# Kernel optimization log

Measured on AMD Instinct MI355X. Metric: run time of the kernel, lower is better.

## Reference

```python
import jax, jax.numpy as jnp
import numpy as np

B, S, D, H = 2, 2048, 1024, 16
HD = D // H

def setup_inputs() -> dict:
    key = jax.random.key(0)
    ks = jax.random.split(key, 6)
    X = jax.random.normal(ks[0], (B, S, D), dtype=jnp.float32)
    mask = jax.random.randint(ks[1], (B, 1, S, S), 0, 2, dtype=jnp.int32)
    scale = 1.0 / np.sqrt(D)
    Wq = jax.random.normal(ks[2], (D, D), dtype=jnp.float32) * scale
    Wk = jax.random.normal(ks[3], (D, D), dtype=jnp.float32) * scale
    Wv = jax.random.normal(ks[4], (D, D), dtype=jnp.float32) * scale
    Wo = jax.random.normal(ks[5], (D, D), dtype=jnp.float32) * scale
    return {"X": X, "mask": mask, "Wq": Wq, "Wk": Wk, "Wv": Wv, "Wo": Wo}

def reference(X, mask, Wq, Wk, Wv, Wo):
    b, s, d = X.shape
    # torch nn.Linear(bias=False): y = x @ W.T, W is [out, in]
    def split_heads(Y):
        return Y.reshape(b, s, H, HD).transpose(0, 2, 1, 3)  # [b,h,s,hd]
    Q = split_heads(X @ Wq.T)
    K = split_heads(X @ Wk.T)
    V = split_heads(X @ Wv.T)
    scores = jnp.einsum('bhqd,bhkd->bhqk', Q, K) / jnp.sqrt(jnp.float32(HD))
    # Faithful to original: masked positions filled with -1e-09 (sic)
    scores = jnp.where(mask == 0, jnp.float32(-1e-09), scores)
    # dropout p=0.0 -> identity (applied to scores pre-softmax in original)
    weights = jax.nn.softmax(scores, axis=-1)
    out = jnp.einsum('bhqk,bhkd->bhqd', weights, V)  # [b,h,s,hd]
    out = out.transpose(0, 2, 1, 3).reshape(b, s, d)
    return out @ Wo.T
```

## Files before the change

### kernel.cpp

```cpp
#include <hip/hip_runtime.h>
#include <hip/hip_bf16.h>

using short8  = __attribute__((ext_vector_type(8))) short;
using short4v = __attribute__((ext_vector_type(4))) short;
using f32x4   = __attribute__((ext_vector_type(4))) float;

#if __has_builtin(__builtin_amdgcn_exp2f)
#define EXP2(x) __builtin_amdgcn_exp2f(x)
#else
#define EXP2(x) __expf(0.6931471805599453f*(x))
#endif

__device__ __forceinline__ unsigned short f2bf(float x){
  union { float f; unsigned u; } c; c.f = x;
  unsigned u = c.u + 0x7FFFu + ((c.u >> 16) & 1u);
  return (unsigned short)(u >> 16);
}

__device__ __forceinline__ unsigned pack_bf16_rn(float a, float b){
  __hip_bfloat162 t = __float22bfloat162_rn(make_float2(a, b));
  unsigned u; __builtin_memcpy(&u, &t, 4);
  return u;
}

__global__ __launch_bounds__(256) void prep(const float* __restrict__ X, const int* __restrict__ Mk,
                                            const float* __restrict__ Wq, const float* __restrict__ Wk,
                                            const float* __restrict__ Wv, const float* __restrict__ Wo,
                                            unsigned short* __restrict__ Xb, unsigned short* __restrict__ Wqkv,
                                            unsigned short* __restrict__ Wob, unsigned long long* __restrict__ Mbits)
{
  const int bid = blockIdx.x, tid = threadIdx.x;
  if (bid < 8192){
    const float* src; unsigned short* dst; float scale; int i;
    if (bid < 4096)      { src = X;  dst = Xb;             scale = 1.0f;          i = bid*1024 + tid*4; }
    else if (bid < 5120) { src = Wq; dst = Wqkv;           scale = 0.18033688f;   i = (bid-4096)*1024 + tid*4; }
    else if (bid < 6144) { src = Wk; dst = Wqkv + 1048576; scale = 1.0f;          i = (bid-5120)*1024 + tid*4; }
    else if (bid < 7168) { src = Wv; dst = Wqkv + 2097152; scale = 1.0f;          i = (bid-6144)*1024 + tid*4; }
    else                 { src = Wo; dst = Wob;            scale = 1.0f;          i = (bid-7168)*1024 + tid*4; }
    float4 v = *(const float4*)(src + i);
    ushort4 o;
    o.x = f2bf(v.x * scale); o.y = f2bf(v.y * scale);
    o.z = f2bf(v.z * scale); o.w = f2bf(v.w * scale);
    *(ushort4*)(dst + i) = o;
  } else {
    int row = bid - 8192;
    const int* src = Mk + (size_t)row * 2048;
    int w = tid >> 6, l = tid & 63;
    #pragma unroll
    for (int p = 0; p < 8; p++){
      int v = src[w*512 + p*64 + l];
      unsigned long long bm = __ballot(v != 0);
      if (l == 0) Mbits[(size_t)(w*8 + p) * 4096 + row] = bm;
    }
  }
}

__device__ __forceinline__ void stage16(const unsigned short* g, unsigned short* l){
  __builtin_amdgcn_global_load_lds(
      (const __attribute__((address_space(1))) void*)g,
      (__attribute__((address_space(3))) void*)l, 16, 0, 0);
}

__global__ __launch_bounds__(256) void gemm_qkv(const unsigned short* __restrict__ A,
                                                const unsigned short* __restrict__ B,
                                                unsigned short* __restrict__ C,
                                                unsigned short* __restrict__ Vg)
{
  __shared__ unsigned short As[128*32];
  __shared__ unsigned short Bs[128*32];
  const int tid = threadIdx.x;
  const int wave = tid >> 6, lane = tid & 63, l16 = lane & 15, quad = lane >> 4;
  const int id = blockIdx.x, xcd = id & 7, m = id >> 3;
  const int bm = (m / 3) * 128, bn = (xcd * 3 + (m % 3)) * 128;
  const int wm = (wave >> 1) * 64, wn = (wave & 1) * 64;
  const int K = 1024;

  f32x4 acc[4][4] = {};
  for (int k0 = 0; k0 < K; k0 += 32){
    #pragma unroll
    for (int c = 0; c < 2; c++){
      int idx = c * 256 + tid;
      int row = idx >> 2, g = (idx & 3) * 8;
      stage16(A + (size_t)(bm + row) * K + k0 + g, &As[idx * 8]);
      stage16(B + (size_t)(bn + row) * K + k0 + g, &Bs[idx * 8]);
    }
    __syncthreads();
    short8 af[4], bf[4];
    #pragma unroll
    for (int i = 0; i < 4; i++) af[i] = *(const short8*)&As[(wm + i*16 + l16)*32 + quad*8];
    #pragma unroll
    for (int j = 0; j < 4; j++) bf[j] = *(const short8*)&Bs[(wn + j*16 + l16)*32 + quad*8];
    #pragma unroll
    for (int i = 0; i < 4; i++)
      #pragma unroll
      for (int j = 0; j < 4; j++)
        acc[i][j] = __builtin_amdgcn_mfma_f32_16x16x32_bf16(af[i], bf[j], acc[i][j], 0, 0, 0);
    __syncthreads();
  }

  if (bn < 2048){
    #pragma unroll
    for (int i = 0; i < 4; i++){
      int mrow = bm + wm + i*16 + quad*4;
      #pragma unroll
      for (int j = 0; j < 4; j++){
        int ncol = bn + wn + j*16 + l16;
        #pragma unroll
        for (int r = 0; r < 4; r++)
          C[(size_t)(mrow + r) * 3072 + ncol] = f2bf(acc[i][j][r]);
      }
    }
  } else {
    #pragma unroll
    for (int i = 0; i < 4; i++){
      int srow = bm + wm + i*16 + quad*4;
      int b = srow >> 11, s = srow & 2047;
      #pragma unroll
      for (int j = 0; j < 4; j++){
        int c = bn - 2048 + wn + j*16 + l16;
        int h = c >> 6, d = c & 63;
        ushort4 o;
        o.x = f2bf(acc[i][j][0]); o.y = f2bf(acc[i][j][1]);
        o.z = f2bf(acc[i][j][2]); o.w = f2bf(acc[i][j][3]);
        *(ushort4*)&Vg[((size_t)(b*16 + h)*64 + d) * 2048 + s] = o;
      }
    }
  }
}

__global__ __launch_bounds__(256) void gemm_out(const unsigned short* __restrict__ A,
                                                const unsigned short* __restrict__ B,
                                                float* __restrict__ Cf)
{
  __shared__ unsigned short As[128*32];
  __shared__ unsigned short Bs[64*32];
  const int tid = threadIdx.x;
  const int wave = tid >> 6, lane = tid & 63, l16 = lane & 15, quad = lane >> 4;
  const int id = blockIdx.x, xcd = id & 7, m = id >> 3;
  const int bm = (m >> 1) * 128, bn = (xcd * 2 + (m & 1)) * 64;
  const int wm = (wave >> 1) * 64, wn = (wave & 1) * 32;
  const int K = 1024, N = 1024;

  f32x4 acc[4][2] = {};
  for (int k0 = 0; k0 < K; k0 += 32){
    #pragma unroll
    for (int c = 0; c < 2; c++){
      int idx = c * 256 + tid;
      int row = idx >> 2, g = (idx & 3) * 8;
      stage16(A + (size_t)(bm + row) * K + k0 + g, &As[idx * 8]);
    }
    stage16(B + (size_t)(bn + (tid >> 2)) * K + k0 + (tid & 3) * 8, &Bs[tid * 8]);
    __syncthreads();
    short8 af[4], bf[2];
    #pragma unroll
    for (int i = 0; i < 4; i++) af[i] = *(const short8*)&As[(wm + i*16 + l16)*32 + quad*8];
    #pragma unroll
    for (int j = 0; j < 2; j++) bf[j] = *(const short8*)&Bs[(wn + j*16 + l16)*32 + quad*8];
    #pragma unroll
    for (int i = 0; i < 4; i++)
      #pragma unroll
      for (int j = 0; j < 2; j++)
        acc[i][j] = __builtin_amdgcn_mfma_f32_16x16x32_bf16(af[i], bf[j], acc[i][j], 0, 0, 0);
    __syncthreads();
  }
  #pragma unroll
  for (int i = 0; i < 4; i++){
    int mrow = bm + wm + i*16 + quad*4;
    #pragma unroll
    for (int j = 0; j < 2; j++){
      int ncol = bn + wn + j*16 + l16;
      #pragma unroll
      for (int r = 0; r < 4; r++)
        Cf[(size_t)(mrow + r) * N + ncol] = acc[i][j][r];
    }
  }
}

__global__ __launch_bounds__(256, 4) void attn(const unsigned short* __restrict__ QKV,
                                               const unsigned short* __restrict__ Vg,
                                               const unsigned long long* __restrict__ Mb,
                                               unsigned short* __restrict__ O)
{
  __shared__ char smem[32768];
  unsigned short* Ks = (unsigned short*)smem;
  unsigned short* Vt = (unsigned short*)(smem + 16384);

  const int tid = threadIdx.x, wave = tid >> 6, lane = tid & 63;
  const int l16 = lane & 15, quad = lane >> 4;
  const int id = blockIdx.x;
  const int xcd = id & 7, m = id >> 3;
  const int bh = xcd * 4 + (m >> 5);
  const int qblk = (m & 31) * 64;
  const int b = bh >> 4, h = bh & 15;
  const unsigned short* Qg  = QKV + (size_t)b * 2048 * 3072 + h * 64;
  const unsigned short* Kg  = Qg + 1024;
  const unsigned short* Vgb = Vg + (size_t)bh * 64 * 2048;

  const int qrow = qblk + wave*16 + l16;
  const unsigned long long* mrow = Mb + (size_t)b*2048 + qrow;

  short8 qf0 = *(const short8*)(Qg + (size_t)qrow * 3072 + quad*8);
  short8 qf1 = *(const short8*)(Qg + (size_t)qrow * 3072 + 32 + quad*8);

  f32x4 oacc[4] = {};
  float plsum = 0.f;
  const int sw = l16 & 7;

  #pragma unroll
  for (int it = 0; it < 2; it++){
    int s = it * 256 + tid;
    int row = s >> 3, bg = (s & 7) ^ (row & 7);
    stage16(Kg + (size_t)row * 3072 + bg * 8, Ks + s * 8);
    stage16(Vgb + (size_t)row * 2048 + bg * 8, Vt + s * 8);
  }
  unsigned long long mcur = mrow[0], mnxt = 0ull;

  for (int c = 0; c < 32; c++){
    const int buf = (c & 1) * 4096;
    __syncthreads();

    if (c < 31){
      const int nj = (c + 1) * 64, nbuf = ((c + 1) & 1) * 4096;
      #pragma unroll
      for (int it = 0; it < 2; it++){
        int s = it * 256 + tid;
        int row = s >> 3, bg = (s & 7) ^ (row & 7);
        stage16(Kg + (size_t)(nj + row) * 3072 + bg * 8, Ks + nbuf + s * 8);
        stage16(Vgb + (size_t)row * 2048 + nj + bg * 8, Vt + nbuf + s * 8);
      }
      mnxt = mrow[(size_t)(c + 1) * 4096];
    }

    #pragma unroll
    for (int kb = 0; kb < 4; kb++){
      const int krow = kb*16 + l16;
      short8 kf0 = *(const short8*)&Ks[buf + krow*64 + ((0 + quad) ^ sw) * 8];
      short8 kf1 = *(const short8*)&Ks[buf + krow*64 + ((4 + quad) ^ sw) * 8];
      f32x4 a = {0.f, 0.f, 0.f, 0.f};
      __builtin_amdgcn_s_setprio(1);
      a = __builtin_amdgcn_mfma_f32_16x16x32_bf16(kf0, qf0, a, 0, 0, 0);
      a = __builtin_amdgcn_mfma_f32_16x16x32_bf16(kf1, qf1, a, 0, 0, 0);
      __builtin_amdgcn_s_setprio(0);
      unsigned mm = (unsigned)(mcur >> (kb*16 + quad*4)) & 15u;
      float p0 = EXP2(a[0]); p0 = (mm & 1u) ? p0 : 1.0f;
      float p1 = EXP2(a[1]); p1 = (mm & 2u) ? p1 : 1.0f;
      float p2 = EXP2(a[2]); p2 = (mm & 4u) ? p2 : 1.0f;
      float p3 = EXP2(a[3]); p3 = (mm & 8u) ? p3 : 1.0f;
      plsum += (p0 + p1) + (p2 + p3);
      uint2 pu; pu.x = pack_bf16_rn(p0, p1); pu.y = pack_bf16_rn(p2, p3);
      short4v pa = *(short4v*)&pu;
      __builtin_amdgcn_s_setprio(1);
      #pragma unroll
      for (int ng = 0; ng < 4; ng++){
        const int vrow = ng*16 + l16;
        short4v vf = *(const short4v*)&Vt[buf + vrow*64 +
                       ((kb*2 + (quad >> 1)) ^ sw) * 8 + (quad & 1) * 4];
        oacc[ng] = __builtin_amdgcn_mfma_f32_16x16x16bf16_1k(pa, vf, oacc[ng], 0, 0, 0);
      }
      __builtin_amdgcn_s_setprio(0);
    }
    mcur = mnxt;
  }

  float v = plsum;
  v += __shfl_xor(v, 16);
  v += __shfl_xor(v, 32);
  float linv = 1.0f / v;
  float lr[4];
  #pragma unroll
  for (int r = 0; r < 4; r++) lr[r] = __shfl(linv, quad*4 + r);

  unsigned short* Ob = O + (size_t)(b*2048 + qblk + wave*16) * 1024 + h*64;
  #pragma unroll
  for (int ng = 0; ng < 4; ng++)
    #pragma unroll
    for (int r = 0; r < 4; r++)
      Ob[(size_t)(quad*4 + r) * 1024 + ng*16 + l16] = f2bf(oacc[ng][r] * lr[r]);
}

extern "C" void kernel_launch(void* const* d_in, const int* in_sizes, int n_in,
                              void* d_out, int out_size, void* d_ws, size_t ws_size,
                              hipStream_t stream)
{
  const float* X  = (const float*)d_in[0];
  const int*   Mk = (const int*)d_in[1];
  const float* Wq = (const float*)d_in[2];
  const float* Wk = (const float*)d_in[3];
  const float* Wv = (const float*)d_in[4];
  const float* Wo = (const float*)d_in[5];
  float* out = (float*)d_out;

  char* ws = (char*)d_ws;
  unsigned short* Xb   = (unsigned short*)(ws + 0);
  unsigned short* Wqkv = (unsigned short*)(ws + 8388608);
  unsigned short* Wob  = (unsigned short*)(ws + 14680064);
  unsigned short* QKV  = (unsigned short*)(ws + 16777216);
  unsigned short* Ob   = (unsigned short*)(ws + 41943040);
  unsigned long long* Mb = (unsigned long long*)(ws + 50331648);
  unsigned short* Vg   = (unsigned short*)(ws + 58720256);

  prep<<<12288, 256, 0, stream>>>(X, Mk, Wq, Wk, Wv, Wo, Xb, Wqkv, Wob, Mb);
  gemm_qkv<<<768, 256, 0, stream>>>(Xb, Wqkv, QKV, Vg);
  attn<<<1024, 256, 0, stream>>>(QKV, Vg, Mb, Ob);
  gemm_out<<<512, 256, 0, stream>>>(Ob, Wob, out);
}
```

Measured before the change: 241.0 us.

## Triple-buffer K/V tiles in attention with prefetch two chunks ahead

The attention kernel moves from double to triple buffering of K and V tiles in shared memory, prefetching the tile two chunks ahead. It replaces __syncthreads with explicit s_waitcnt on vmcnt plus a raw barrier, so the newest loads can stay in flight. It also drops the s_setprio hints and lowers launch bounds from 4 to 3 blocks per CU, since shared memory grows to 48KB. The aim is to hide global-load latency, at the cost of fewer resident blocks. The hand-counted vmcnt value depends on how the compiler lowers stage16 and the mask load.

```diff
diff --git a/kernel.cpp b/kernel.cpp
--- a/kernel.cpp
+++ b/kernel.cpp
@@ -176,14 +176,14 @@
   }
 }
 
-__global__ __launch_bounds__(256, 4) void attn(const unsigned short* __restrict__ QKV,
+__global__ __launch_bounds__(256, 3) void attn(const unsigned short* __restrict__ QKV,
                                                const unsigned short* __restrict__ Vg,
                                                const unsigned long long* __restrict__ Mb,
                                                unsigned short* __restrict__ O)
 {
-  __shared__ char smem[32768];
+  __shared__ char smem[49152];
   unsigned short* Ks = (unsigned short*)smem;
-  unsigned short* Vt = (unsigned short*)(smem + 16384);
+  unsigned short* Vt = (unsigned short*)(smem + 24576);
 
   const int tid = threadIdx.x, wave = tid >> 6, lane = tid & 63;
   const int l16 = lane & 15, quad = lane >> 4;
@@ -206,41 +206,52 @@
   float plsum = 0.f;
   const int sw = l16 & 7;
 
-  #pragma unroll
-  for (int it = 0; it < 2; it++){
-    int s = it * 256 + tid;
-    int row = s >> 3, bg = (s & 7) ^ (row & 7);
-    stage16(Kg + (size_t)row * 3072 + bg * 8, Ks + s * 8);
-    stage16(Vgb + (size_t)row * 2048 + bg * 8, Vt + s * 8);
-  }
-  unsigned long long mcur = mrow[0], mnxt = 0ull;
-
+  const int s0 = tid, s1 = 256 + tid;
+  const int row0 = s0 >> 3, bg0 = (s0 & 7) ^ (row0 & 7);
+  const int row1 = s1 >> 3, bg1 = (s1 & 7) ^ (row1 & 7);
+
+  stage16(Kg  + (size_t)row0 * 3072 + bg0 * 8,      Ks + s0 * 8);
+  stage16(Vgb + (size_t)row0 * 2048 + bg0 * 8,      Vt + s0 * 8);
+  stage16(Kg  + (size_t)row1 * 3072 + bg1 * 8,      Ks + s1 * 8);
+  stage16(Vgb + (size_t)row1 * 2048 + bg1 * 8,      Vt + s1 * 8);
+  stage16(Kg  + (size_t)(64 + row0) * 3072 + bg0 * 8, Ks + 4096 + s0 * 8);
+  stage16(Vgb + (size_t)row0 * 2048 + 64 + bg0 * 8,   Vt + 4096 + s0 * 8);
+  stage16(Kg  + (size_t)(64 + row1) * 3072 + bg1 * 8, Ks + 4096 + s1 * 8);
+  stage16(Vgb + (size_t)row1 * 2048 + 64 + bg1 * 8,   Vt + 4096 + s1 * 8);
+  unsigned long long mcur = mrow[0];
+  unsigned long long mnxt = mrow[4096];
+  unsigned long long mnn  = 0ull;
+
+  int sc = 0;
   for (int c = 0; c < 32; c++){
-    const int buf = (c & 1) * 4096;
-    __syncthreads();
-
-    if (c < 31){
-      const int nj = (c + 1) * 64, nbuf = ((c + 1) & 1) * 4096;
-      #pragma unroll
-      for (int it = 0; it < 2; it++){
-        int s = it * 256 + tid;
-        int row = s >> 3, bg = (s & 7) ^ (row & 7);
-        stage16(Kg + (size_t)(nj + row) * 3072 + bg * 8, Ks + nbuf + s * 8);
-        stage16(Vgb + (size_t)row * 2048 + nj + bg * 8, Vt + nbuf + s * 8);
-      }
-      mnxt = mrow[(size_t)(c + 1) * 4096];
-    }
-
+    if (c == 0 || c == 31){
+      __asm__ volatile("s_waitcnt vmcnt(0) lgkmcnt(0)" ::: "memory");
+    } else {
+      __asm__ volatile("s_waitcnt vmcnt(5) lgkmcnt(0)" ::: "memory");
+    }
+    __builtin_amdgcn_s_barrier();
+    __builtin_amdgcn_sched_barrier(0);
+
+    if (c < 30){
+      int s2 = sc + 2; if (s2 >= 3) s2 -= 3;
+      const int nj = (c + 2) * 64;
+      const int kb2 = s2 * 4096;
+      stage16(Kg  + (size_t)(nj + row0) * 3072 + bg0 * 8, Ks + kb2 + s0 * 8);
+      stage16(Vgb + (size_t)row0 * 2048 + nj + bg0 * 8,   Vt + kb2 + s0 * 8);
+      stage16(Kg  + (size_t)(nj + row1) * 3072 + bg1 * 8, Ks + kb2 + s1 * 8);
+      stage16(Vgb + (size_t)row1 * 2048 + nj + bg1 * 8,   Vt + kb2 + s1 * 8);
+      mnn = mrow[(size_t)(c + 2) * 4096];
+    }
+
+    const int buf = sc * 4096;
     #pragma unroll
     for (int kb = 0; kb < 4; kb++){
       const int krow = kb*16 + l16;
       short8 kf0 = *(const short8*)&Ks[buf + krow*64 + ((0 + quad) ^ sw) * 8];
       short8 kf1 = *(const short8*)&Ks[buf + krow*64 + ((4 + quad) ^ sw) * 8];
       f32x4 a = {0.f, 0.f, 0.f, 0.f};
-      __builtin_amdgcn_s_setprio(1);
       a = __builtin_amdgcn_mfma_f32_16x16x32_bf16(kf0, qf0, a, 0, 0, 0);
       a = __builtin_amdgcn_mfma_f32_16x16x32_bf16(kf1, qf1, a, 0, 0, 0);
-      __builtin_amdgcn_s_setprio(0);
       unsigned mm = (unsigned)(mcur >> (kb*16 + quad*4)) & 15u;
       float p0 = EXP2(a[0]); p0 = (mm & 1u) ? p0 : 1.0f;
       float p1 = EXP2(a[1]); p1 = (mm & 2u) ? p1 : 1.0f;
@@ -249,7 +260,6 @@
       plsum += (p0 + p1) + (p2 + p3);
       uint2 pu; pu.x = pack_bf16_rn(p0, p1); pu.y = pack_bf16_rn(p2, p3);
       short4v pa = *(short4v*)&pu;
-      __builtin_amdgcn_s_setprio(1);
       #pragma unroll
       for (int ng = 0; ng < 4; ng++){
         const int vrow = ng*16 + l16;
@@ -257,9 +267,9 @@
                        ((kb*2 + (quad >> 1)) ^ sw) * 8 + (quad & 1) * 4];
         oacc[ng] = __builtin_amdgcn_mfma_f32_16x16x16bf16_1k(pa, vf, oacc[ng], 0, 0, 0);
       }
-      __builtin_amdgcn_s_setprio(0);
-    }
-    mcur = mnxt;
+    }
+    mcur = mnxt; mnxt = mnn;
+    sc += 1; if (sc == 3) sc = 0;
   }
 
   float v = plsum;
```

New measurement: 261.1 us. 8.3% more time.

## Split attention key range across two wave groups and reduce partial outputs in LDS

Applied to the files above, without the earlier changes.

The attention block grows to 512 threads. Two groups of four waves each cover half of the key sequence for the same 64 query rows, staging 32-key chunks with their own double buffers and a new V swizzle. The partial outputs and row sums are then combined through shared memory before normalisation and the store. The setprio hints are removed. The aim is more waves in flight per query tile to hide latency, at the cost of an extra LDS reduction and a block barrier per smaller chunk.

```diff
diff --git a/kernel.cpp b/kernel.cpp
--- a/kernel.cpp
+++ b/kernel.cpp
@@ -176,7 +176,7 @@
   }
 }
 
-__global__ __launch_bounds__(256, 4) void attn(const unsigned short* __restrict__ QKV,
+__global__ __launch_bounds__(512, 8) void attn(const unsigned short* __restrict__ QKV,
                                                const unsigned short* __restrict__ Vg,
                                                const unsigned long long* __restrict__ Mb,
                                                unsigned short* __restrict__ O)
@@ -187,6 +187,8 @@
 
   const int tid = threadIdx.x, wave = tid >> 6, lane = tid & 63;
   const int l16 = lane & 15, quad = lane >> 4;
+  const int st = tid >> 8;
+  const int wlocal = wave & 3;
   const int id = blockIdx.x;
   const int xcd = id & 7, m = id >> 3;
   const int bh = xcd * 4 + (m >> 5);
@@ -195,9 +197,10 @@
   const unsigned short* Qg  = QKV + (size_t)b * 2048 * 3072 + h * 64;
   const unsigned short* Kg  = Qg + 1024;
   const unsigned short* Vgb = Vg + (size_t)bh * 64 * 2048;
-
-  const int qrow = qblk + wave*16 + l16;
-  const unsigned long long* mrow = Mb + (size_t)b*2048 + qrow;
+  const unsigned* Mb32 = (const unsigned*)Mb;
+
+  const int qrow = qblk + wlocal*16 + l16;
+  const int mrowi = (b*2048 + qrow) * 2;
 
   short8 qf0 = *(const short8*)(Qg + (size_t)qrow * 3072 + quad*8);
   short8 qf1 = *(const short8*)(Qg + (size_t)qrow * 3072 + 32 + quad*8);
@@ -206,42 +209,37 @@
   float plsum = 0.f;
   const int sw = l16 & 7;
 
-  #pragma unroll
-  for (int it = 0; it < 2; it++){
-    int s = it * 256 + tid;
-    int row = s >> 3, bg = (s & 7) ^ (row & 7);
-    stage16(Kg + (size_t)row * 3072 + bg * 8, Ks + s * 8);
-    stage16(Vgb + (size_t)row * 2048 + bg * 8, Vt + s * 8);
-  }
-  unsigned long long mcur = mrow[0], mnxt = 0ull;
+  const int t = tid & 255;
+  const int rowK = t >> 3, bgK = (t & 7) ^ (rowK & 7);
+  const int rowV = t >> 2, bgV = (t & 3) ^ ((rowV >> 1) & 3);
+  const int kbase = st * 1024;
+
+  stage16(Kg  + (size_t)(kbase + rowK) * 3072 + bgK * 8,   Ks + (st*2 + 0) * 2048 + t * 8);
+  stage16(Vgb + (size_t)rowV * 2048 + kbase + bgV * 8,     Vt + (st*2 + 0) * 2048 + t * 8);
+  unsigned mcur = Mb32[(size_t)(st*16) * 8192 + mrowi];
+  unsigned mnxt = 0u;
 
   for (int c = 0; c < 32; c++){
-    const int buf = (c & 1) * 4096;
     __syncthreads();
 
     if (c < 31){
-      const int nj = (c + 1) * 64, nbuf = ((c + 1) & 1) * 4096;
-      #pragma unroll
-      for (int it = 0; it < 2; it++){
-        int s = it * 256 + tid;
-        int row = s >> 3, bg = (s & 7) ^ (row & 7);
-        stage16(Kg + (size_t)(nj + row) * 3072 + bg * 8, Ks + nbuf + s * 8);
-        stage16(Vgb + (size_t)row * 2048 + nj + bg * 8, Vt + nbuf + s * 8);
-      }
-      mnxt = mrow[(size_t)(c + 1) * 4096];
-    }
-
-    #pragma unroll
-    for (int kb = 0; kb < 4; kb++){
+      const int cj = c + 1, so = (st*2 + (cj & 1)) * 2048;
+      const int kj = kbase + cj * 32;
+      stage16(Kg  + (size_t)(kj + rowK) * 3072 + bgK * 8, Ks + so + t * 8);
+      stage16(Vgb + (size_t)rowV * 2048 + kj + bgV * 8,   Vt + so + t * 8);
+      mnxt = Mb32[(size_t)(st*16 + (cj >> 1)) * 8192 + mrowi + (cj & 1)];
+    }
+
+    const int bufo = (st*2 + (c & 1)) * 2048;
+    #pragma unroll
+    for (int kb = 0; kb < 2; kb++){
       const int krow = kb*16 + l16;
-      short8 kf0 = *(const short8*)&Ks[buf + krow*64 + ((0 + quad) ^ sw) * 8];
-      short8 kf1 = *(const short8*)&Ks[buf + krow*64 + ((4 + quad) ^ sw) * 8];
+      short8 kf0 = *(const short8*)&Ks[bufo + krow*64 + ((0 + quad) ^ sw) * 8];
+      short8 kf1 = *(const short8*)&Ks[bufo + krow*64 + ((4 + quad) ^ sw) * 8];
       f32x4 a = {0.f, 0.f, 0.f, 0.f};
-      __builtin_amdgcn_s_setprio(1);
       a = __builtin_amdgcn_mfma_f32_16x16x32_bf16(kf0, qf0, a, 0, 0, 0);
       a = __builtin_amdgcn_mfma_f32_16x16x32_bf16(kf1, qf1, a, 0, 0, 0);
-      __builtin_amdgcn_s_setprio(0);
-      unsigned mm = (unsigned)(mcur >> (kb*16 + quad*4)) & 15u;
+      unsigned mm = (mcur >> (kb*16 + quad*4)) & 15u;
       float p0 = EXP2(a[0]); p0 = (mm & 1u) ? p0 : 1.0f;
       float p1 = EXP2(a[1]); p1 = (mm & 2u) ? p1 : 1.0f;
       float p2 = EXP2(a[2]); p2 = (mm & 4u) ? p2 : 1.0f;
@@ -249,33 +247,51 @@
       plsum += (p0 + p1) + (p2 + p3);
       uint2 pu; pu.x = pack_bf16_rn(p0, p1); pu.y = pack_bf16_rn(p2, p3);
       short4v pa = *(short4v*)&pu;
-      __builtin_amdgcn_s_setprio(1);
       #pragma unroll
       for (int ng = 0; ng < 4; ng++){
         const int vrow = ng*16 + l16;
-        short4v vf = *(const short4v*)&Vt[buf + vrow*64 +
-                       ((kb*2 + (quad >> 1)) ^ sw) * 8 + (quad & 1) * 4];
+        const int phys8 = (kb*2 + (quad >> 1)) ^ ((vrow >> 1) & 3);
+        short4v vf = *(const short4v*)&Vt[bufo + vrow*32 + phys8*8 + (quad & 1) * 4];
         oacc[ng] = __builtin_amdgcn_mfma_f32_16x16x16bf16_1k(pa, vf, oacc[ng], 0, 0, 0);
       }
-      __builtin_amdgcn_s_setprio(0);
     }
     mcur = mnxt;
   }
 
-  float v = plsum;
-  v += __shfl_xor(v, 16);
-  v += __shfl_xor(v, 32);
-  float linv = 1.0f / v;
-  float lr[4];
-  #pragma unroll
-  for (int r = 0; r < 4; r++) lr[r] = __shfl(linv, quad*4 + r);
-
-  unsigned short* Ob = O + (size_t)(b*2048 + qblk + wave*16) * 1024 + h*64;
-  #pragma unroll
-  for (int ng = 0; ng < 4; ng++)
-    #pragma unroll
-    for (int r = 0; r < 4; r++)
-      Ob[(size_t)(quad*4 + r) * 1024 + ng*16 + l16] = f2bf(oacc[ng][r] * lr[r]);
+  float* fb = (float*)smem;
+  __syncthreads();
+  if (st == 1){
+    const int o = (wlocal*64 + lane) * 17;
+    #pragma unroll
+    for (int ng = 0; ng < 4; ng++)
+      #pragma unroll
+      for (int r = 0; r < 4; r++) fb[o + ng*4 + r] = oacc[ng][r];
+    fb[o + 16] = plsum;
+  }
+  __syncthreads();
+  if (st == 0){
+    const int o = (wlocal*64 + lane) * 17;
+    #pragma unroll
+    for (int ng = 0; ng < 4; ng++)
+      #pragma unroll
+      for (int r = 0; r < 4; r++) oacc[ng][r] += fb[o + ng*4 + r];
+    plsum += fb[o + 16];
+
+    float v = plsum;
+    v += __shfl_xor(v, 16);
+    v += __shfl_xor(v, 32);
+    float linv = 1.0f / v;
+    float lr[4];
+    #pragma unroll
+    for (int r = 0; r < 4; r++) lr[r] = __shfl(linv, quad*4 + r);
+
+    unsigned short* Ob = O + (size_t)(b*2048 + qblk + wlocal*16) * 1024 + h*64;
+    #pragma unroll
+    for (int ng = 0; ng < 4; ng++)
+      #pragma unroll
+      for (int r = 0; r < 4; r++)
+        Ob[(size_t)(quad*4 + r) * 1024 + ng*16 + l16] = f2bf(oacc[ng][r] * lr[r]);
+  }
 }
 
 extern "C" void kernel_launch(void* const* d_in, const int* in_sizes, int n_in,
@@ -301,6 +317,6 @@
 
   prep<<<12288, 256, 0, stream>>>(X, Mk, Wq, Wk, Wv, Wo, Xb, Wqkv, Wob, Mb);
   gemm_qkv<<<768, 256, 0, stream>>>(Xb, Wqkv, QKV, Vg);
-  attn<<<1024, 256, 0, stream>>>(QKV, Vg, Mb, Ob);
+  attn<<<1024, 512, 0, stream>>>(QKV, Vg, Mb, Ob);
   gemm_out<<<512, 256, 0, stream>>>(Ob, Wob, out);
 }
```

New measurement: 242.5 us. No clear change (+0.6%).
